# Kernel optimization log

Measured on AMD Instinct MI355X. Metric: run time of the kernel, lower is better.

Reference implementation:

```python
import jax, jax.numpy as jnp
import numpy as np
import math

B, S, D, H = 2, 2048, 1024, 16
DK = D // H


def setup_inputs() -> dict:
    key = jax.random.key(0)
    ks = jax.random.split(key, 12)
    scale = 1.0 / math.sqrt(D)
    inp = {
        'query': jax.random.normal(ks[0], (B, S, D), dtype=jnp.float32),
        'key': jax.random.normal(ks[1], (B, S, D), dtype=jnp.float32),
        'value': jax.random.normal(ks[2], (B, S, D), dtype=jnp.float32),
        'mask': jnp.ones((B, 1, S), dtype=jnp.int32),
        'posr': jax.random.normal(ks[3], (B, S, S), dtype=jnp.float32),
        'Wq': jax.random.normal(ks[4], (D, D), dtype=jnp.float32) * scale,
        'bq': jnp.zeros((D,), dtype=jnp.float32),
        'Wk': jax.random.normal(ks[5], (D, D), dtype=jnp.float32) * scale,
        'bk': jnp.zeros((D,), dtype=jnp.float32),
        'Wv': jax.random.normal(ks[6], (D, D), dtype=jnp.float32) * scale,
        'bv': jnp.zeros((D,), dtype=jnp.float32),
        'Wo': jax.random.normal(ks[7], (D, D), dtype=jnp.float32) * scale,
        'bo': jnp.zeros((D,), dtype=jnp.float32),
    }
    return inp


def _split_heads(x):
    # [B, S, D] -> [B, H, S, DK]
    b, s, _ = x.shape
    return x.reshape(b, s, H, DK).transpose(0, 2, 1, 3)


def reference(query, key, value, mask, posr, Wq, bq, Wk, bk, Wv, bv, Wo, bo):
    q = _split_heads(query @ Wq.T + bq)   # [B,H,S,DK]
    k = _split_heads(key @ Wk.T + bk)
    v = _split_heads(value @ Wv.T + bv)

    scores = jnp.einsum('bhqd,bhkd->bhqk', q, k) / math.sqrt(DK)
    scores = scores + posr[:, None, :, :]            # additive positional bias
    m = mask[:, None, :, :]                           # [B,1,1,S] broadcast
    scores = jnp.where(m == 0, jnp.float32(-1e9), scores)
    p = jax.nn.softmax(scores, axis=-1)
    ctx = jnp.einsum('bhqk,bhkd->bhqd', p, v)        # [B,H,S,DK]
    ctx = ctx.transpose(0, 2, 1, 3).reshape(query.shape[0], -1, D)
    return ctx @ Wo.T + bo
```

## Files before the change

kernel.cpp:

```cpp
#include <hip/hip_runtime.h>
#include <math.h>

#define B_ 2
#define S_ 2048
#define D_ 1024
#define H_ 16
#define DK_ 64

typedef __attribute__((ext_vector_type(8))) short bf16x8;
typedef __attribute__((ext_vector_type(4))) float f32x4;

#define MFMA16(a, b, c) __builtin_amdgcn_mfma_f32_16x16x32_bf16((a), (b), (c), 0, 0, 0)

#define ASYNC16(g, l)                                                          \
    __builtin_amdgcn_global_load_lds(                                          \
        (const __attribute__((address_space(1))) void*)(g),                    \
        (__attribute__((address_space(3))) void*)(l), 16, 0, 0)

__device__ __forceinline__ unsigned short f2bf(float x) {
    unsigned int u = __float_as_uint(x);
    unsigned int r = (u + 0x7fffu + ((u >> 16) & 1u)) >> 16;
    return (unsigned short)r;
}

__global__ __launch_bounds__(256)
void pack_all(const float* __restrict__ q, const float* __restrict__ k,
              const float* __restrict__ v, const float* __restrict__ wq,
              const float* __restrict__ wk, const float* __restrict__ wv,
              const float* __restrict__ wo, unsigned short* __restrict__ ws0)
{
    const int z = blockIdx.z;
    const size_t IN = 4194304, WT = 1048576;
    const float* in;
    unsigned short* dst;
    int n;
    switch (z) {
        case 0: in = q;  dst = ws0;            n = (int)IN; break;
        case 1: in = k;  dst = ws0 + IN;       n = (int)IN; break;
        case 2: in = v;  dst = ws0 + 2*IN;     n = (int)IN; break;
        case 3: in = wq; dst = ws0 + 3*IN;          n = (int)WT; break;
        case 4: in = wk; dst = ws0 + 3*IN + WT;     n = (int)WT; break;
        case 5: in = wv; dst = ws0 + 3*IN + 2*WT;   n = (int)WT; break;
        default:in = wo; dst = ws0 + 3*IN + 3*WT;   n = (int)WT; break;
    }
    const int n4 = n >> 2;
    const int stride = gridDim.x * blockDim.x;
    for (int i = blockIdx.x * blockDim.x + threadIdx.x; i < n4; i += stride) {
        float4 x = ((const float4*)in)[i];
        ushort4 hv;
        hv.x = f2bf(x.x); hv.y = f2bf(x.y); hv.z = f2bf(x.z); hv.w = f2bf(x.w);
        ((ushort4*)dst)[i] = hv;
    }
}

__device__ __forceinline__ void gemm_core(
    const unsigned short* __restrict__ A, const unsigned short* __restrict__ B,
    unsigned short* As, unsigned short* Bs, int m0, int n0, f32x4 (&acc)[4][4])
{
    const int tid  = threadIdx.x;
    const int w    = tid >> 6;
    const int lane = tid & 63;
    const int rA   = lane & 15;
    const int quad = lane >> 4;
    const int wm   = (w & 1) * 64;
    const int wn   = (w >> 1) * 64;

#pragma unroll 1
    for (int k0 = 0; k0 < 1024; k0 += 64) {
        __syncthreads();
#pragma unroll
        for (int i = 0; i < 4; ++i) {
            const int c   = i * 256 + tid;
            const int row = c >> 3;
            const int g   = (c & 7) ^ (row & 7);
            ASYNC16(A + (size_t)(m0 + row) * 1024 + k0 + g * 8,
                    As + (size_t)(i * 256 + w * 64) * 8);
            ASYNC16(B + (size_t)(n0 + row) * 1024 + k0 + g * 8,
                    Bs + (size_t)(i * 256 + w * 64) * 8);
        }
        __syncthreads();
#pragma unroll
        for (int ks = 0; ks < 2; ++ks) {
            bf16x8 a[4], bb[4];
#pragma unroll
            for (int mt = 0; mt < 4; ++mt) {
                const int row = wm + mt * 16 + rA;
                a[mt] = *(const bf16x8*)&As[row * 64 + (((ks * 4 + quad) ^ (row & 7)) * 8)];
            }
#pragma unroll
            for (int nt = 0; nt < 4; ++nt) {
                const int row = wn + nt * 16 + rA;
                bb[nt] = *(const bf16x8*)&Bs[row * 64 + (((ks * 4 + quad) ^ (row & 7)) * 8)];
            }
#pragma unroll
            for (int mt = 0; mt < 4; ++mt)
#pragma unroll
                for (int nt = 0; nt < 4; ++nt)
                    acc[mt][nt] = MFMA16(a[mt], bb[nt], acc[mt][nt]);
        }
    }
}

__global__ __launch_bounds__(256)
void gemm_qkv(const unsigned short* __restrict__ ws0,
              const float* __restrict__ bq, const float* __restrict__ bk,
              const float* __restrict__ bv,
              unsigned short* __restrict__ qbuf, unsigned short* __restrict__ kbuf,
              unsigned short* __restrict__ vtbuf)
{
    __shared__ unsigned short As[128 * 64];
    __shared__ unsigned short Bs[128 * 64];
    const size_t IN = 4194304, WT = 1048576;
    const int z = blockIdx.z;
    const unsigned short* Ap = ws0 + (size_t)z * IN;
    const unsigned short* Bp = ws0 + 3 * IN + (size_t)z * WT;
    const float* bias = (z == 0) ? bq : (z == 1) ? bk : bv;
    unsigned short* dst = (z == 0) ? qbuf : (z == 1) ? kbuf : vtbuf;

    const int m0 = blockIdx.y * 128;
    const int n0 = blockIdx.x * 128;
    f32x4 acc[4][4] = {};
    gemm_core(Ap, Bp, As, Bs, m0, n0, acc);

    const int tid = threadIdx.x, w = tid >> 6, lane = tid & 63;
    const int quad = lane >> 4, col = lane & 15;
    const int wm = (w & 1) * 64, wn = (w >> 1) * 64;
    const float qscale = (z == 0) ? 0.125f : 1.0f;
#pragma unroll
    for (int mt = 0; mt < 4; ++mt)
#pragma unroll
        for (int nt = 0; nt < 4; ++nt) {
            f32x4 v = acc[mt][nt];
#pragma unroll
            for (int r = 0; r < 4; ++r) {
                const int m = m0 + wm + mt * 16 + quad * 4 + r;
                const int n = n0 + wn + nt * 16 + col;
                const float val = (v[r] + bias[n]) * qscale;
                const int bb = m >> 11, ss = m & 2047;
                const int hh = n >> 6, dd = n & 63;
                if (z == 2)
                    dst[((size_t)(bb * 16 + hh) * 64 + dd) * 2048 + ss] = f2bf(val);
                else
                    dst[((size_t)(bb * 16 + hh) * 2048 + ss) * 64 + dd] = f2bf(val);
            }
        }
}

__global__ __launch_bounds__(256)
void gemm_out(const unsigned short* __restrict__ Actx,
              const unsigned short* __restrict__ Bwo,
              const float* __restrict__ bias, float* __restrict__ out)
{
    __shared__ unsigned short As[128 * 64];
    __shared__ unsigned short Bs[128 * 64];
    const int m0 = blockIdx.y * 128;
    const int n0 = blockIdx.x * 128;
    f32x4 acc[4][4] = {};
    gemm_core(Actx, Bwo, As, Bs, m0, n0, acc);

    const int tid = threadIdx.x, w = tid >> 6, lane = tid & 63;
    const int quad = lane >> 4, col = lane & 15;
    const int wm = (w & 1) * 64, wn = (w >> 1) * 64;
#pragma unroll
    for (int mt = 0; mt < 4; ++mt)
#pragma unroll
        for (int nt = 0; nt < 4; ++nt) {
            f32x4 v = acc[mt][nt];
#pragma unroll
            for (int r = 0; r < 4; ++r) {
                const int m = m0 + wm + mt * 16 + quad * 4 + r;
                const int n = n0 + wn + nt * 16 + col;
                out[(size_t)m * 1024 + n] = v[r] + bias[n];
            }
        }
}

__global__ __launch_bounds__(512, 4)
void attn_mfma(const unsigned short* __restrict__ qbuf,
               const unsigned short* __restrict__ kbuf,
               const unsigned short* __restrict__ vtbuf,
               const float* __restrict__ posr, const int* __restrict__ mask,
               unsigned short* __restrict__ ctxb)
{
    __shared__ unsigned short Ks[2][64 * 64];
    __shared__ unsigned short Vts[2][64 * 64];
    __shared__ unsigned short Ps[128 * 64];

    const int tid  = threadIdx.x;
    const int w    = tid >> 6;
    const int lane = tid & 63;
    const int quad = lane >> 4;
    const int col  = lane & 15;
    const int q0   = blockIdx.x * 128;
    const int h    = blockIdx.y;
    const int b    = blockIdx.z;
    const int wq   = w * 16;

    const size_t headoff = (size_t)(b * 16 + h) * 2048 * 64;
    const unsigned short* Qh  = qbuf + headoff + (size_t)q0 * 64;
    const unsigned short* Kh  = kbuf + headoff;
    const unsigned short* Vth = vtbuf + headoff;

    const int srow = tid >> 3;
    const int sg   = (tid & 7) ^ (srow & 7);

    bf16x8 qf[2];
#pragma unroll
    for (int ks = 0; ks < 2; ++ks)
        qf[ks] = *(const bf16x8*)&Qh[(size_t)(wq + col) * 64 + ks * 32 + quad * 8];

    ASYNC16(Kh + (size_t)srow * 64 + sg * 8,   &Ks[0][(size_t)(w * 64) * 8]);
    ASYNC16(Vth + (size_t)srow * 2048 + sg * 8, &Vts[0][(size_t)(w * 64) * 8]);

    f32x4 O[4] = {};
    float lsum[4] = {0.f, 0.f, 0.f, 0.f};

    const float* prp[4];
#pragma unroll
    for (int r = 0; r < 4; ++r)
        prp[r] = posr + ((size_t)b * 2048 + (q0 + wq + quad * 4 + r)) * 2048;
    const int* mrow = mask + (size_t)b * 2048;

#pragma unroll 1
    for (int t = 0; t < 32; ++t) {
        __syncthreads();
        const int bb = t & 1;
        const int k0 = t * 64;
        if (t + 1 < 32) {
            const int kn = k0 + 64;
            ASYNC16(Kh + (size_t)(kn + srow) * 64 + sg * 8,   &Ks[bb ^ 1][(size_t)(w * 64) * 8]);
            ASYNC16(Vth + (size_t)srow * 2048 + kn + sg * 8,  &Vts[bb ^ 1][(size_t)(w * 64) * 8]);
        }

        int mk[4];
#pragma unroll
        for (int nt = 0; nt < 4; ++nt) mk[nt] = mrow[k0 + nt * 16 + col];
        float pr[4][4];
#pragma unroll
        for (int r = 0; r < 4; ++r)
#pragma unroll
            for (int nt = 0; nt < 4; ++nt)
                pr[r][nt] = prp[r][k0 + nt * 16 + col];

        f32x4 sc[4] = {};
#pragma unroll
        for (int ks = 0; ks < 2; ++ks) {
#pragma unroll
            for (int nt = 0; nt < 4; ++nt) {
                const bf16x8 bk = *(const bf16x8*)
                    &Ks[bb][(nt * 16 + col) * 64 + (((ks * 4 + quad) ^ (col & 7)) * 8)];
                sc[nt] = MFMA16(qf[ks], bk, sc[nt]);
            }
        }

#pragma unroll
        for (int r = 0; r < 4; ++r) {
            const int rowW = wq + quad * 4 + r;
            const int rsw = rowW & 7;
#pragma unroll
            for (int nt = 0; nt < 4; ++nt) {
                float p = __expf(sc[nt][r] + pr[r][nt]);
                p = mk[nt] ? p : 0.f;
                lsum[r] += p;
                const int kk = nt * 16 + col;
                Ps[rowW * 64 + (((kk >> 3) ^ rsw) * 8) + (kk & 7)] = f2bf(p);
            }
        }

#pragma unroll
        for (int ks = 0; ks < 2; ++ks) {
            const bf16x8 ap = *(const bf16x8*)
                &Ps[(wq + col) * 64 + (((ks * 4 + quad) ^ (col & 7)) * 8)];
#pragma unroll
            for (int nt = 0; nt < 4; ++nt) {
                const bf16x8 bv = *(const bf16x8*)
                    &Vts[bb][(nt * 16 + col) * 64 + (((ks * 4 + quad) ^ (col & 7)) * 8)];
                O[nt] = MFMA16(ap, bv, O[nt]);
            }
        }
    }

#pragma unroll
    for (int r = 0; r < 4; ++r) {
#pragma unroll
        for (int o = 1; o < 16; o <<= 1) lsum[r] += __shfl_xor(lsum[r], o);
    }

#pragma unroll
    for (int r = 0; r < 4; ++r) {
        const float inv = 1.f / lsum[r];
        const size_t rowoff = ((size_t)b * 2048 + (q0 + wq + quad * 4 + r)) * 1024 + h * 64;
#pragma unroll
        for (int nt = 0; nt < 4; ++nt)
            ctxb[rowoff + nt * 16 + col] = f2bf(O[nt][r] * inv);
    }
}

extern "C" void kernel_launch(void* const* d_in, const int* in_sizes, int n_in,
                              void* d_out, int out_size, void* d_ws, size_t ws_size,
                              hipStream_t stream) {
    const float* query = (const float*)d_in[0];
    const float* key   = (const float*)d_in[1];
    const float* value = (const float*)d_in[2];
    const int*   mask  = (const int*)  d_in[3];
    const float* posr  = (const float*)d_in[4];
    const float* Wq    = (const float*)d_in[5];
    const float* bq    = (const float*)d_in[6];
    const float* Wk    = (const float*)d_in[7];
    const float* bk    = (const float*)d_in[8];
    const float* Wv    = (const float*)d_in[9];
    const float* bv    = (const float*)d_in[10];
    const float* Wo    = (const float*)d_in[11];
    const float* bo    = (const float*)d_in[12];
    float* out = (float*)d_out;

    unsigned short* ws0   = (unsigned short*)d_ws;
    const size_t IN = 4194304, WT = 1048576;
    unsigned short* qbuf  = ws0 + 4 * IN;
    unsigned short* kbuf  = ws0 + 5 * IN;
    unsigned short* vtbuf = ws0 + 6 * IN;
    unsigned short* ctxb  = ws0 + 7 * IN;
    const unsigned short* wob = ws0 + 3 * IN + 3 * WT;

    pack_all<<<dim3(512, 1, 7), 256, 0, stream>>>(query, key, value, Wq, Wk, Wv, Wo, ws0);

    gemm_qkv<<<dim3(8, 32, 3), 256, 0, stream>>>(ws0, bq, bk, bv, qbuf, kbuf, vtbuf);

    attn_mfma<<<dim3(16, 16, 2), 512, 0, stream>>>(qbuf, kbuf, vtbuf, posr, mask, ctxb);

    gemm_out<<<dim3(8, 32), 256, 0, stream>>>(ctxb, wob, bo, out);
}
```

Measured before the change: 306.8 us.

## Pipeline attention with triple-buffered K/V and 512-thread GEMMs

```diff
diff --git a/kernel.cpp b/kernel.cpp
--- a/kernel.cpp
+++ b/kernel.cpp
@@ -16,6 +16,8 @@
     __builtin_amdgcn_global_load_lds(                                          \
         (const __attribute__((address_space(1))) void*)(g),                    \
         (__attribute__((address_space(3))) void*)(l), 16, 0, 0)
+
+#define LOG2E 1.4426950408889634f
 
 __device__ __forceinline__ unsigned short f2bf(float x) {
     unsigned int u = __float_as_uint(x);
@@ -53,9 +55,9 @@
     }
 }
 
-__device__ __forceinline__ void gemm_core(
+__device__ __forceinline__ void gemm_core512(
     const unsigned short* __restrict__ A, const unsigned short* __restrict__ B,
-    unsigned short* As, unsigned short* Bs, int m0, int n0, f32x4 (&acc)[4][4])
+    unsigned short* As, unsigned short* Bs, int m0, int n0, f32x4 (&acc)[4][2])
 {
     const int tid  = threadIdx.x;
     const int w    = tid >> 6;
@@ -63,45 +65,45 @@
     const int rA   = lane & 15;
     const int quad = lane >> 4;
     const int wm   = (w & 1) * 64;
-    const int wn   = (w >> 1) * 64;
+    const int wn   = (w >> 1) * 32;
 
 #pragma unroll 1
     for (int k0 = 0; k0 < 1024; k0 += 64) {
         __syncthreads();
 #pragma unroll
-        for (int i = 0; i < 4; ++i) {
-            const int c   = i * 256 + tid;
+        for (int i = 0; i < 2; ++i) {
+            const int c   = i * 512 + tid;
             const int row = c >> 3;
             const int g   = (c & 7) ^ (row & 7);
             ASYNC16(A + (size_t)(m0 + row) * 1024 + k0 + g * 8,
-                    As + (size_t)(i * 256 + w * 64) * 8);
+                    As + (size_t)(i * 512 + w * 64) * 8);
             ASYNC16(B + (size_t)(n0 + row) * 1024 + k0 + g * 8,
-                    Bs + (size_t)(i * 256 + w * 64) * 8);
+                    Bs + (size_t)(i * 512 + w * 64) * 8);
         }
         __syncthreads();
 #pragma unroll
         for (int ks = 0; ks < 2; ++ks) {
-            bf16x8 a[4], bb[4];
+            bf16x8 a[4], bb2[2];
 #pragma unroll
             for (int mt = 0; mt < 4; ++mt) {
                 const int row = wm + mt * 16 + rA;
                 a[mt] = *(const bf16x8*)&As[row * 64 + (((ks * 4 + quad) ^ (row & 7)) * 8)];
             }
 #pragma unroll
-            for (int nt = 0; nt < 4; ++nt) {
+            for (int nt = 0; nt < 2; ++nt) {
                 const int row = wn + nt * 16 + rA;
-                bb[nt] = *(const bf16x8*)&Bs[row * 64 + (((ks * 4 + quad) ^ (row & 7)) * 8)];
+                bb2[nt] = *(const bf16x8*)&Bs[row * 64 + (((ks * 4 + quad) ^ (row & 7)) * 8)];
             }
 #pragma unroll
             for (int mt = 0; mt < 4; ++mt)
 #pragma unroll
-                for (int nt = 0; nt < 4; ++nt)
-                    acc[mt][nt] = MFMA16(a[mt], bb[nt], acc[mt][nt]);
-        }
-    }
-}
-
-__global__ __launch_bounds__(256)
+                for (int nt = 0; nt < 2; ++nt)
+                    acc[mt][nt] = MFMA16(a[mt], bb2[nt], acc[mt][nt]);
+        }
+    }
+}
+
+__global__ __launch_bounds__(512, 4)
 void gemm_qkv(const unsigned short* __restrict__ ws0,
               const float* __restrict__ bq, const float* __restrict__ bk,
               const float* __restrict__ bv,
@@ -119,17 +121,17 @@
 
     const int m0 = blockIdx.y * 128;
     const int n0 = blockIdx.x * 128;
-    f32x4 acc[4][4] = {};
-    gemm_core(Ap, Bp, As, Bs, m0, n0, acc);
+    f32x4 acc[4][2] = {};
+    gemm_core512(Ap, Bp, As, Bs, m0, n0, acc);
 
     const int tid = threadIdx.x, w = tid >> 6, lane = tid & 63;
     const int quad = lane >> 4, col = lane & 15;
-    const int wm = (w & 1) * 64, wn = (w >> 1) * 64;
-    const float qscale = (z == 0) ? 0.125f : 1.0f;
+    const int wm = (w & 1) * 64, wn = (w >> 1) * 32;
+    const float qscale = (z == 0) ? (0.125f * LOG2E) : 1.0f;
 #pragma unroll
     for (int mt = 0; mt < 4; ++mt)
 #pragma unroll
-        for (int nt = 0; nt < 4; ++nt) {
+        for (int nt = 0; nt < 2; ++nt) {
             f32x4 v = acc[mt][nt];
 #pragma unroll
             for (int r = 0; r < 4; ++r) {
@@ -146,7 +148,7 @@
         }
 }
 
-__global__ __launch_bounds__(256)
+__global__ __launch_bounds__(512, 4)
 void gemm_out(const unsigned short* __restrict__ Actx,
               const unsigned short* __restrict__ Bwo,
               const float* __restrict__ bias, float* __restrict__ out)
@@ -155,16 +157,16 @@
     __shared__ unsigned short Bs[128 * 64];
     const int m0 = blockIdx.y * 128;
     const int n0 = blockIdx.x * 128;
-    f32x4 acc[4][4] = {};
-    gemm_core(Actx, Bwo, As, Bs, m0, n0, acc);
+    f32x4 acc[4][2] = {};
+    gemm_core512(Actx, Bwo, As, Bs, m0, n0, acc);
 
     const int tid = threadIdx.x, w = tid >> 6, lane = tid & 63;
     const int quad = lane >> 4, col = lane & 15;
-    const int wm = (w & 1) * 64, wn = (w >> 1) * 64;
+    const int wm = (w & 1) * 64, wn = (w >> 1) * 32;
 #pragma unroll
     for (int mt = 0; mt < 4; ++mt)
 #pragma unroll
-        for (int nt = 0; nt < 4; ++nt) {
+        for (int nt = 0; nt < 2; ++nt) {
             f32x4 v = acc[mt][nt];
 #pragma unroll
             for (int r = 0; r < 4; ++r) {
@@ -182,8 +184,8 @@
                const float* __restrict__ posr, const int* __restrict__ mask,
                unsigned short* __restrict__ ctxb)
 {
-    __shared__ unsigned short Ks[2][64 * 64];
-    __shared__ unsigned short Vts[2][64 * 64];
+    __shared__ unsigned short Ks[3][64 * 64];
+    __shared__ unsigned short Vts[3][64 * 64];
     __shared__ unsigned short Ps[128 * 64];
 
     const int tid  = threadIdx.x;
@@ -209,63 +211,71 @@
     for (int ks = 0; ks < 2; ++ks)
         qf[ks] = *(const bf16x8*)&Qh[(size_t)(wq + col) * 64 + ks * 32 + quad * 8];
 
-    ASYNC16(Kh + (size_t)srow * 64 + sg * 8,   &Ks[0][(size_t)(w * 64) * 8]);
+    ASYNC16(Kh + (size_t)srow * 64 + sg * 8,    &Ks[0][(size_t)(w * 64) * 8]);
     ASYNC16(Vth + (size_t)srow * 2048 + sg * 8, &Vts[0][(size_t)(w * 64) * 8]);
 
     f32x4 O[4] = {};
     float lsum[4] = {0.f, 0.f, 0.f, 0.f};
 
-    const float* prp[4];
+    const float* prq[4];
 #pragma unroll
     for (int r = 0; r < 4; ++r)
-        prp[r] = posr + ((size_t)b * 2048 + (q0 + wq + quad * 4 + r)) * 2048;
+        prq[r] = posr + ((size_t)b * 2048 + (q0 + wq + quad * 4 + r)) * 2048;
     const int* mrow = mask + (size_t)b * 2048;
 
+    float pr[4][4];
+#pragma unroll
+    for (int r = 0; r < 4; ++r)
+#pragma unroll
+        for (int nt = 0; nt < 4; ++nt)
+            pr[r][nt] = prq[r][nt * 16 + col];
+
+    __syncthreads();
+
+    f32x4 sc[4] = {};
+#pragma unroll
+    for (int ks = 0; ks < 2; ++ks)
+#pragma unroll
+        for (int nt = 0; nt < 4; ++nt) {
+            const bf16x8 bk = *(const bf16x8*)
+                &Ks[0][(nt * 16 + col) * 64 + (((ks * 4 + quad) ^ (col & 7)) * 8)];
+            sc[nt] = MFMA16(qf[ks], bk, sc[nt]);
+        }
+
+    int bb = 0;
 #pragma unroll 1
     for (int t = 0; t < 32; ++t) {
-        __syncthreads();
-        const int bb = t & 1;
         const int k0 = t * 64;
-        if (t + 1 < 32) {
+        const int bn = (bb == 2) ? 0 : bb + 1;
+
+        int mk[4];
+#pragma unroll
+        for (int nt = 0; nt < 4; ++nt) mk[nt] = mrow[k0 + nt * 16 + col];
+
+        if (t < 31) {
             const int kn = k0 + 64;
-            ASYNC16(Kh + (size_t)(kn + srow) * 64 + sg * 8,   &Ks[bb ^ 1][(size_t)(w * 64) * 8]);
-            ASYNC16(Vth + (size_t)srow * 2048 + kn + sg * 8,  &Vts[bb ^ 1][(size_t)(w * 64) * 8]);
-        }
-
-        int mk[4];
-#pragma unroll
-        for (int nt = 0; nt < 4; ++nt) mk[nt] = mrow[k0 + nt * 16 + col];
-        float pr[4][4];
-#pragma unroll
-        for (int r = 0; r < 4; ++r)
-#pragma unroll
-            for (int nt = 0; nt < 4; ++nt)
-                pr[r][nt] = prp[r][k0 + nt * 16 + col];
-
-        f32x4 sc[4] = {};
-#pragma unroll
-        for (int ks = 0; ks < 2; ++ks) {
-#pragma unroll
-            for (int nt = 0; nt < 4; ++nt) {
-                const bf16x8 bk = *(const bf16x8*)
-                    &Ks[bb][(nt * 16 + col) * 64 + (((ks * 4 + quad) ^ (col & 7)) * 8)];
-                sc[nt] = MFMA16(qf[ks], bk, sc[nt]);
-            }
+            ASYNC16(Kh + (size_t)(kn + srow) * 64 + sg * 8,  &Ks[bn][(size_t)(w * 64) * 8]);
+            ASYNC16(Vth + (size_t)srow * 2048 + kn + sg * 8, &Vts[bn][(size_t)(w * 64) * 8]);
         }
 
 #pragma unroll
         for (int r = 0; r < 4; ++r) {
             const int rowW = wq + quad * 4 + r;
-            const int rsw = rowW & 7;
+            const int rsw  = rowW & 7;
 #pragma unroll
             for (int nt = 0; nt < 4; ++nt) {
-                float p = __expf(sc[nt][r] + pr[r][nt]);
-                p = mk[nt] ? p : 0.f;
-                lsum[r] += p;
+                const float e = __builtin_amdgcn_exp2f(
+                    fmaf(pr[r][nt], LOG2E, sc[nt][r]));
+                unsigned int u = __float_as_uint(e) & 0xffff0000u;
+                u = mk[nt] ? u : 0u;
+                lsum[r] += __uint_as_float(u);
                 const int kk = nt * 16 + col;
-                Ps[rowW * 64 + (((kk >> 3) ^ rsw) * 8) + (kk & 7)] = f2bf(p);
-            }
-        }
+                Ps[rowW * 64 + ((((kk >> 3) ^ rsw)) * 8) + (kk & 7)] =
+                    (unsigned short)(u >> 16);
+            }
+        }
+
+        if (t < 31) __syncthreads();
 
 #pragma unroll
         for (int ks = 0; ks < 2; ++ks) {
@@ -273,11 +283,31 @@
                 &Ps[(wq + col) * 64 + (((ks * 4 + quad) ^ (col & 7)) * 8)];
 #pragma unroll
             for (int nt = 0; nt < 4; ++nt) {
-                const bf16x8 bv = *(const bf16x8*)
+                const bf16x8 vb = *(const bf16x8*)
                     &Vts[bb][(nt * 16 + col) * 64 + (((ks * 4 + quad) ^ (col & 7)) * 8)];
-                O[nt] = MFMA16(ap, bv, O[nt]);
-            }
-        }
+                O[nt] = MFMA16(ap, vb, O[nt]);
+            }
+        }
+
+        if (t < 31) {
+            const int kn = k0 + 64;
+#pragma unroll
+            for (int r = 0; r < 4; ++r)
+#pragma unroll
+                for (int nt = 0; nt < 4; ++nt)
+                    pr[r][nt] = prq[r][kn + nt * 16 + col];
+#pragma unroll
+            for (int nt = 0; nt < 4; ++nt) sc[nt] = (f32x4){0.f, 0.f, 0.f, 0.f};
+#pragma unroll
+            for (int ks = 0; ks < 2; ++ks)
+#pragma unroll
+                for (int nt = 0; nt < 4; ++nt) {
+                    const bf16x8 bk = *(const bf16x8*)
+                        &Ks[bn][(nt * 16 + col) * 64 + (((ks * 4 + quad) ^ (col & 7)) * 8)];
+                    sc[nt] = MFMA16(qf[ks], bk, sc[nt]);
+                }
+        }
+        bb = bn;
     }
 
 #pragma unroll
@@ -324,9 +354,9 @@
 
     pack_all<<<dim3(512, 1, 7), 256, 0, stream>>>(query, key, value, Wq, Wk, Wv, Wo, ws0);
 
-    gemm_qkv<<<dim3(8, 32, 3), 256, 0, stream>>>(ws0, bq, bk, bv, qbuf, kbuf, vtbuf);
+    gemm_qkv<<<dim3(8, 32, 3), 512, 0, stream>>>(ws0, bq, bk, bv, qbuf, kbuf, vtbuf);
 
     attn_mfma<<<dim3(16, 16, 2), 512, 0, stream>>>(qbuf, kbuf, vtbuf, posr, mask, ctxb);
 
-    gemm_out<<<dim3(8, 32), 256, 0, stream>>>(ctxb, wob, bo, out);
-}
+    gemm_out<<<dim3(8, 32), 512, 0, stream>>>(ctxb, wob, bo, out);
+}
```

Result: faster. 273.3 us (-10.9%).
